# Optimization experiments

Hardware: AMD Instinct MI355X
Metric: run time of the kernel (lower is better)

The kernel has to match this reference:

```python
import jax, jax.numpy as jnp
from jax import lax
import numpy as np

B, T, I, H = 64, 2048, 256, 512


def setup_inputs() -> dict:
    key = jax.random.key(0)
    ks = jax.random.split(key, 5)
    stdv = 1.0 / np.sqrt(H)
    return {
        "x": jax.random.normal(ks[0], (B, T, I), dtype=jnp.float32),
        "w_ih0": jax.random.normal(ks[1], (H, I), dtype=jnp.float32) * 0.01,
        "w_hh0": jax.random.uniform(ks[2], (H,), dtype=jnp.float32, minval=-stdv, maxval=stdv),
        "b_ih0": jnp.zeros((H,), dtype=jnp.float32),
        "w_ih1": jax.random.normal(ks[3], (H, H), dtype=jnp.float32) * 0.01,
        "w_hh1": jax.random.uniform(ks[4], (H,), dtype=jnp.float32, minval=-stdv, maxval=stdv),
        "b_ih1": jnp.zeros((H,), dtype=jnp.float32),
    }


def _indrnn_layer(inp, w_ih, w_hh, b_ih):
    # Precompute input projection for all timesteps in one GEMM
    # (identical math to per-step F.linear). pre: (B, T, H)
    pre = jnp.einsum("bti,hi->bth", inp, w_ih) + b_ih
    h0 = jnp.zeros((inp.shape[0], w_hh.shape[0]), dtype=inp.dtype)

    def step(h, p_t):  # p_t: (B, H)
        h = jax.nn.relu(p_t + w_hh * h)
        return h, h

    _, ys = lax.scan(step, h0, jnp.swapaxes(pre, 0, 1))  # ys: (T, B, H)
    return jnp.swapaxes(ys, 0, 1)  # (B, T, H)


def reference(x, w_ih0, w_hh0, b_ih0, w_ih1, w_hh1, b_ih1):
    out = _indrnn_layer(x, w_ih0, w_hh0, b_ih0)
    out = _indrnn_layer(out, w_ih1, w_hh1, b_ih1)
    return out  # torch module returns (out, None); out.squeeze(2) is a no-op for H>1
```

## Files before the change

kernel.cpp:

```cpp
#include <hip/hip_runtime.h>
#include <hip/hip_bf16.h>


#define BB 64
#define TT 2048
#define II 256
#define HH 512
#define MM (BB * TT)

typedef __attribute__((ext_vector_type(8))) short bf16x8;
typedef __attribute__((ext_vector_type(4))) float f32x4;

__device__ inline unsigned short bf16_rne(float f) {
  unsigned u = __builtin_bit_cast(unsigned, f);
  u += 0x7FFFu + ((u >> 16) & 1u);
  return (unsigned short)(u >> 16);
}
__device__ inline float bf16_val(unsigned short h) {
  unsigned u = ((unsigned)h) << 16;
  return __builtin_bit_cast(float, u);
}

template <int K>
__global__ __launch_bounds__(256) void gemm_mfma(const float* __restrict__ A,
                                                 const float* __restrict__ W,
                                                 const float* __restrict__ bias,
                                                 float* __restrict__ C) {
  constexpr int BM = 128, BN = 128, BK = 32;
  constexpr int LDT = 40;
  __shared__ unsigned short Ah[BM * LDT], Al[BM * LDT];
  __shared__ unsigned short Bh[BN * LDT], Bl[BN * LDT];

  const int bid = blockIdx.x;
  const int xcd = bid & 7;
  const int local = bid >> 3;
  const int mb = xcd * (MM / BM / 8) + (local >> 2);
  const int nb = local & 3;
  const int m0 = mb * BM, n0 = nb * BN;

  const int tid = threadIdx.x;
  const int lane = tid & 63;
  const int wave = tid >> 6;
  const int wr = wave >> 1, wc = wave & 1;
  const int lrow = lane & 15, lkg = lane >> 4;

  f32x4 acc[4][4] = {};

  const int srow = tid >> 1;
  const int skq = (tid & 1) * 4;

  for (int kt = 0; kt < K; kt += BK) {
    const float4* Aq = (const float4*)(A + (size_t)(m0 + srow) * K + kt) + skq;
    const float4* Wq = (const float4*)(W + (size_t)(n0 + srow) * K + kt) + skq;
    float4 av[4], wv[4];
#pragma unroll
    for (int s = 0; s < 4; ++s) { av[s] = Aq[s]; wv[s] = Wq[s]; }

    __syncthreads();

#pragma unroll
    for (int s = 0; s < 4; ++s) {
      const int kk = (skq + s) * 4;
      const float fa[4] = {av[s].x, av[s].y, av[s].z, av[s].w};
      const float fw[4] = {wv[s].x, wv[s].y, wv[s].z, wv[s].w};
      ushort4 ah, al, wh, wl;
      unsigned short* pah = (unsigned short*)&ah;
      unsigned short* pal = (unsigned short*)&al;
      unsigned short* pwh = (unsigned short*)&wh;
      unsigned short* pwl = (unsigned short*)&wl;
#pragma unroll
      for (int e = 0; e < 4; ++e) {
        const unsigned short h1 = bf16_rne(fa[e]);
        pah[e] = h1;
        pal[e] = bf16_rne(fa[e] - bf16_val(h1));
        const unsigned short h2 = bf16_rne(fw[e]);
        pwh[e] = h2;
        pwl[e] = bf16_rne(fw[e] - bf16_val(h2));
      }
      *(ushort4*)&Ah[srow * LDT + kk] = ah;
      *(ushort4*)&Al[srow * LDT + kk] = al;
      *(ushort4*)&Bh[srow * LDT + kk] = wh;
      *(ushort4*)&Bl[srow * LDT + kk] = wl;
    }
    __syncthreads();

    bf16x8 afh[4], afl[4], bfh[4], bfl[4];
#pragma unroll
    for (int i = 0; i < 4; ++i) {
      const int ar = wr * 64 + i * 16 + lrow;
      afh[i] = *(const bf16x8*)&Ah[ar * LDT + lkg * 8];
      afl[i] = *(const bf16x8*)&Al[ar * LDT + lkg * 8];
      const int br = wc * 64 + i * 16 + lrow;
      bfh[i] = *(const bf16x8*)&Bh[br * LDT + lkg * 8];
      bfl[i] = *(const bf16x8*)&Bl[br * LDT + lkg * 8];
    }
#pragma unroll
    for (int i = 0; i < 4; ++i)
#pragma unroll
      for (int j = 0; j < 4; ++j) {
        acc[i][j] = __builtin_amdgcn_mfma_f32_16x16x32_bf16(afh[i], bfh[j], acc[i][j], 0, 0, 0);
        acc[i][j] = __builtin_amdgcn_mfma_f32_16x16x32_bf16(afh[i], bfl[j], acc[i][j], 0, 0, 0);
        acc[i][j] = __builtin_amdgcn_mfma_f32_16x16x32_bf16(afl[i], bfh[j], acc[i][j], 0, 0, 0);
      }
  }

  const int rb = (lane >> 4) * 4;
#pragma unroll
  for (int j = 0; j < 4; ++j) {
    const int col = n0 + wc * 64 + j * 16 + lrow;
    const float bv = bias[col];
#pragma unroll
    for (int i = 0; i < 4; ++i) {
      const int row0 = m0 + wr * 64 + i * 16 + rb;
#pragma unroll
      for (int r = 0; r < 4; ++r)
        C[(size_t)(row0 + r) * HH + col] = acc[i][j][r] + bv;
    }
  }
}

__global__ __launch_bounds__(256, 1) void indrnn_scan(float* __restrict__ buf,
                                                      const float* __restrict__ w_hh) {
  const int gid = blockIdx.x * 256 + threadIdx.x;
  const int b = gid >> 9;
  const int h = gid & 511;
  const float w = w_hh[h];
  float* p = buf + (size_t)b * TT * HH + h;

  constexpr int U = 64;
  float cur[U], nxt[U];
  float hv = 0.f;

#pragma unroll
  for (int u = 0; u < U; ++u) cur[u] = p[(size_t)u * HH];

  for (int t0 = 0; t0 < TT; t0 += U) {
    const bool more = (t0 + U) < TT;
    if (more) {
#pragma unroll
      for (int u = 0; u < U; ++u) nxt[u] = p[(size_t)(t0 + U + u) * HH];
    }
#pragma unroll
    for (int u = 0; u < U; ++u) {
      hv = fmaxf(fmaf(w, hv, cur[u]), 0.f);
      cur[u] = hv;
    }
#pragma unroll
    for (int u = 0; u < U; ++u) p[(size_t)(t0 + u) * HH] = cur[u];
    if (more) {
#pragma unroll
      for (int u = 0; u < U; ++u) cur[u] = nxt[u];
    }
  }
}

extern "C" void kernel_launch(void* const* d_in, const int* in_sizes, int n_in,
                              void* d_out, int out_size, void* d_ws, size_t ws_size,
                              hipStream_t stream) {
  const float* x     = (const float*)d_in[0];
  const float* w_ih0 = (const float*)d_in[1];
  const float* w_hh0 = (const float*)d_in[2];
  const float* b_ih0 = (const float*)d_in[3];
  const float* w_ih1 = (const float*)d_in[4];
  const float* w_hh1 = (const float*)d_in[5];
  const float* b_ih1 = (const float*)d_in[6];
  float* out = (float*)d_out;
  float* ws  = (float*)d_ws;

  const int ntiles = (MM / 128) * (HH / 128);

  gemm_mfma<II><<<ntiles, 256, 0, stream>>>(x, w_ih0, b_ih0, ws);
  indrnn_scan<<<(BB * HH) / 256, 256, 0, stream>>>(ws, w_hh0);
  gemm_mfma<HH><<<ntiles, 256, 0, stream>>>(ws, w_ih1, b_ih1, out);
  indrnn_scan<<<(BB * HH) / 256, 256, 0, stream>>>(out, w_hh1);
}
```

Before: 1.022 ms.

## Pre-split weights and layer-1 activations to bf16 hi/lo; async LDS-prefetch scan

Adds a kernel that converts the weights once into bf16 high/low halves, and makes the first scan emit its output directly as bf16 high/low pairs, so the second GEMM loads pre-split operands instead of converting fp32 in every tile. The scan is rewritten as 64-thread blocks that stream the pre-activations into LDS with global_load_lds and several chunks in flight. This removes the per-tile conversion ALU work and fp32 loads, at the cost of extra workspace, two small launches, and writing two 16-bit arrays instead of one fp32 array. A fallback path runs when the workspace is too small.

```diff
diff --git a/kernel.cpp b/kernel.cpp
--- a/kernel.cpp
+++ b/kernel.cpp
@@ -21,11 +21,18 @@
   return __builtin_bit_cast(float, u);
 }
 
-template <int K>
-__global__ __launch_bounds__(256) void gemm_mfma(const float* __restrict__ A,
-                                                 const float* __restrict__ W,
-                                                 const float* __restrict__ bias,
-                                                 float* __restrict__ C) {
+typedef __attribute__((address_space(1))) const void GASV;
+typedef __attribute__((address_space(3))) void LASV;
+__device__ inline void gload_lds4(const float* g, float* l) {
+  __builtin_amdgcn_global_load_lds((GASV*)g, (LASV*)l, 4, 0, 0);
+}
+
+template <int K, int MODE>
+__global__ __launch_bounds__(256) void gemm_mfma(
+    const float* __restrict__ Af, const unsigned short* __restrict__ Ahg,
+    const unsigned short* __restrict__ Alg, const float* __restrict__ Wf,
+    const unsigned short* __restrict__ Whg, const unsigned short* __restrict__ Wlg,
+    const float* __restrict__ bias, float* __restrict__ C) {
   constexpr int BM = 128, BN = 128, BK = 32;
   constexpr int LDT = 40;
   __shared__ unsigned short Ah[BM * LDT], Al[BM * LDT];
@@ -48,39 +55,81 @@
 
   const int srow = tid >> 1;
   const int skq = (tid & 1) * 4;
+  const int skq8 = (tid & 1) * 16;
 
   for (int kt = 0; kt < K; kt += BK) {
-    const float4* Aq = (const float4*)(A + (size_t)(m0 + srow) * K + kt) + skq;
-    const float4* Wq = (const float4*)(W + (size_t)(n0 + srow) * K + kt) + skq;
     float4 av[4], wv[4];
-#pragma unroll
-    for (int s = 0; s < 4; ++s) { av[s] = Aq[s]; wv[s] = Wq[s]; }
+    bf16x8 a8[4], w8[4];
+    if constexpr (MODE == 2) {
+      const size_t ro = (size_t)(m0 + srow) * K + kt + skq8;
+      a8[0] = *(const bf16x8*)(Ahg + ro);
+      a8[1] = *(const bf16x8*)(Ahg + ro + 8);
+      a8[2] = *(const bf16x8*)(Alg + ro);
+      a8[3] = *(const bf16x8*)(Alg + ro + 8);
+    } else {
+      const float4* Aq = (const float4*)(Af + (size_t)(m0 + srow) * K + kt) + skq;
+#pragma unroll
+      for (int s = 0; s < 4; ++s) av[s] = Aq[s];
+    }
+    if constexpr (MODE >= 1) {
+      const size_t ro = (size_t)(n0 + srow) * K + kt + skq8;
+      w8[0] = *(const bf16x8*)(Whg + ro);
+      w8[1] = *(const bf16x8*)(Whg + ro + 8);
+      w8[2] = *(const bf16x8*)(Wlg + ro);
+      w8[3] = *(const bf16x8*)(Wlg + ro + 8);
+    } else {
+      const float4* Wq = (const float4*)(Wf + (size_t)(n0 + srow) * K + kt) + skq;
+#pragma unroll
+      for (int s = 0; s < 4; ++s) wv[s] = Wq[s];
+    }
 
     __syncthreads();
 
-#pragma unroll
-    for (int s = 0; s < 4; ++s) {
-      const int kk = (skq + s) * 4;
-      const float fa[4] = {av[s].x, av[s].y, av[s].z, av[s].w};
-      const float fw[4] = {wv[s].x, wv[s].y, wv[s].z, wv[s].w};
-      ushort4 ah, al, wh, wl;
-      unsigned short* pah = (unsigned short*)&ah;
-      unsigned short* pal = (unsigned short*)&al;
-      unsigned short* pwh = (unsigned short*)&wh;
-      unsigned short* pwl = (unsigned short*)&wl;
-#pragma unroll
-      for (int e = 0; e < 4; ++e) {
-        const unsigned short h1 = bf16_rne(fa[e]);
-        pah[e] = h1;
-        pal[e] = bf16_rne(fa[e] - bf16_val(h1));
-        const unsigned short h2 = bf16_rne(fw[e]);
-        pwh[e] = h2;
-        pwl[e] = bf16_rne(fw[e] - bf16_val(h2));
-      }
-      *(ushort4*)&Ah[srow * LDT + kk] = ah;
-      *(ushort4*)&Al[srow * LDT + kk] = al;
-      *(ushort4*)&Bh[srow * LDT + kk] = wh;
-      *(ushort4*)&Bl[srow * LDT + kk] = wl;
+    if constexpr (MODE == 2) {
+      *(bf16x8*)&Ah[srow * LDT + skq8] = a8[0];
+      *(bf16x8*)&Ah[srow * LDT + skq8 + 8] = a8[1];
+      *(bf16x8*)&Al[srow * LDT + skq8] = a8[2];
+      *(bf16x8*)&Al[srow * LDT + skq8 + 8] = a8[3];
+    } else {
+#pragma unroll
+      for (int s = 0; s < 4; ++s) {
+        const int kk = (skq + s) * 4;
+        const float fa[4] = {av[s].x, av[s].y, av[s].z, av[s].w};
+        ushort4 ah4, al4;
+        unsigned short* pah = (unsigned short*)&ah4;
+        unsigned short* pal = (unsigned short*)&al4;
+#pragma unroll
+        for (int e = 0; e < 4; ++e) {
+          const unsigned short h1 = bf16_rne(fa[e]);
+          pah[e] = h1;
+          pal[e] = bf16_rne(fa[e] - bf16_val(h1));
+        }
+        *(ushort4*)&Ah[srow * LDT + kk] = ah4;
+        *(ushort4*)&Al[srow * LDT + kk] = al4;
+      }
+    }
+    if constexpr (MODE >= 1) {
+      *(bf16x8*)&Bh[srow * LDT + skq8] = w8[0];
+      *(bf16x8*)&Bh[srow * LDT + skq8 + 8] = w8[1];
+      *(bf16x8*)&Bl[srow * LDT + skq8] = w8[2];
+      *(bf16x8*)&Bl[srow * LDT + skq8 + 8] = w8[3];
+    } else {
+#pragma unroll
+      for (int s = 0; s < 4; ++s) {
+        const int kk = (skq + s) * 4;
+        const float fw[4] = {wv[s].x, wv[s].y, wv[s].z, wv[s].w};
+        ushort4 wh4, wl4;
+        unsigned short* pwh = (unsigned short*)&wh4;
+        unsigned short* pwl = (unsigned short*)&wl4;
+#pragma unroll
+        for (int e = 0; e < 4; ++e) {
+          const unsigned short h2 = bf16_rne(fw[e]);
+          pwh[e] = h2;
+          pwl[e] = bf16_rne(fw[e] - bf16_val(h2));
+        }
+        *(ushort4*)&Bh[srow * LDT + kk] = wh4;
+        *(ushort4*)&Bl[srow * LDT + kk] = wl4;
+      }
     }
     __syncthreads();
 
@@ -119,38 +168,62 @@
   }
 }
 
-__global__ __launch_bounds__(256, 1) void indrnn_scan(float* __restrict__ buf,
-                                                      const float* __restrict__ w_hh) {
-  const int gid = blockIdx.x * 256 + threadIdx.x;
-  const int b = gid >> 9;
-  const int h = gid & 511;
+template <bool SPLIT>
+__global__ __launch_bounds__(64) void indrnn_scan2(
+    const float* __restrict__ pre, const float* __restrict__ w_hh,
+    float* __restrict__ outf, unsigned short* __restrict__ outh,
+    unsigned short* __restrict__ outl) {
+  constexpr int CH = 16, NCH = TT / CH, AHEAD = 3;
+  __shared__ float lds[4 * CH * 64];
+  const int lane = threadIdx.x;
+  const int gid = blockIdx.x * 64 + lane;
+  const int h = gid & (HH - 1);
+  const size_t colbase = (size_t)(gid >> 9) * TT * HH + h;
+
   const float w = w_hh[h];
-  float* p = buf + (size_t)b * TT * HH + h;
-
-  constexpr int U = 64;
-  float cur[U], nxt[U];
   float hv = 0.f;
 
-#pragma unroll
-  for (int u = 0; u < U; ++u) cur[u] = p[(size_t)u * HH];
-
-  for (int t0 = 0; t0 < TT; t0 += U) {
-    const bool more = (t0 + U) < TT;
-    if (more) {
-#pragma unroll
-      for (int u = 0; u < U; ++u) nxt[u] = p[(size_t)(t0 + U + u) * HH];
-    }
-#pragma unroll
-    for (int u = 0; u < U; ++u) {
-      hv = fmaxf(fmaf(w, hv, cur[u]), 0.f);
-      cur[u] = hv;
-    }
-#pragma unroll
-    for (int u = 0; u < U; ++u) p[(size_t)(t0 + u) * HH] = cur[u];
-    if (more) {
-#pragma unroll
-      for (int u = 0; u < U; ++u) cur[u] = nxt[u];
-    }
+  auto issue = [&](int c) {
+    const float* g = pre + colbase + (size_t)(c * CH) * HH;
+    float* l = &lds[(c & 3) * CH * 64];
+#pragma unroll
+    for (int tt = 0; tt < CH; ++tt) gload_lds4(g + (size_t)tt * HH, l + tt * 64);
+  };
+
+  issue(0);
+  issue(1);
+  issue(2);
+  for (int c = 0; c < NCH; ++c) {
+    if (c + AHEAD < NCH) issue(c + AHEAD);
+    asm volatile("s_waitcnt vmcnt(48)" ::: "memory");
+    __builtin_amdgcn_sched_barrier(0);
+    const float* l = &lds[(c & 3) * CH * 64];
+#pragma unroll
+    for (int tt = 0; tt < CH; ++tt) {
+      const float p = l[tt * 64 + lane];
+      hv = fmaxf(fmaf(w, hv, p), 0.f);
+      const size_t gi = colbase + (size_t)(c * CH + tt) * HH;
+      if constexpr (SPLIT) {
+        const unsigned short hh = bf16_rne(hv);
+        outh[gi] = hh;
+        outl[gi] = bf16_rne(hv - bf16_val(hh));
+      } else {
+        outf[gi] = hv;
+      }
+    }
+  }
+}
+
+__global__ __launch_bounds__(256) void convert_w(const float* __restrict__ W,
+                                                 unsigned short* __restrict__ Wh,
+                                                 unsigned short* __restrict__ Wl,
+                                                 int n) {
+  const int i = blockIdx.x * 256 + threadIdx.x;
+  if (i < n) {
+    const float f = W[i];
+    const unsigned short hh = bf16_rne(f);
+    Wh[i] = hh;
+    Wl[i] = bf16_rne(f - bf16_val(hh));
   }
 }
 
@@ -165,12 +238,37 @@
   const float* w_hh1 = (const float*)d_in[5];
   const float* b_ih1 = (const float*)d_in[6];
   float* out = (float*)d_out;
-  float* ws  = (float*)d_ws;
+  float* pre0 = (float*)d_ws;
+  char* wsb = (char*)d_ws;
+
+  const size_t OFF_A1H = 268435456ull;
+  const size_t OFF_A1L = OFF_A1H + 134217728ull;
+  const size_t OFF_W0H = OFF_A1L + 134217728ull;
+  const size_t OFF_W0L = OFF_W0H + 262144ull;
+  const size_t OFF_W1H = OFF_W0L + 262144ull;
+  const size_t OFF_W1L = OFF_W1H + 524288ull;
+  const size_t NEED = OFF_W1L + 524288ull;
 
   const int ntiles = (MM / 128) * (HH / 128);
 
-  gemm_mfma<II><<<ntiles, 256, 0, stream>>>(x, w_ih0, b_ih0, ws);
-  indrnn_scan<<<(BB * HH) / 256, 256, 0, stream>>>(ws, w_hh0);
-  gemm_mfma<HH><<<ntiles, 256, 0, stream>>>(ws, w_ih1, b_ih1, out);
-  indrnn_scan<<<(BB * HH) / 256, 256, 0, stream>>>(out, w_hh1);
-}
+  if (ws_size >= NEED) {
+    unsigned short* A1h = (unsigned short*)(wsb + OFF_A1H);
+    unsigned short* A1l = (unsigned short*)(wsb + OFF_A1L);
+    unsigned short* W0h = (unsigned short*)(wsb + OFF_W0H);
+    unsigned short* W0l = (unsigned short*)(wsb + OFF_W0L);
+    unsigned short* W1h = (unsigned short*)(wsb + OFF_W1H);
+    unsigned short* W1l = (unsigned short*)(wsb + OFF_W1L);
+
+    convert_w<<<(HH * II) / 256, 256, 0, stream>>>(w_ih0, W0h, W0l, HH * II);
+    convert_w<<<(HH * HH) / 256, 256, 0, stream>>>(w_ih1, W1h, W1l, HH * HH);
+    gemm_mfma<II, 1><<<ntiles, 256, 0, stream>>>(x, nullptr, nullptr, nullptr, W0h, W0l, b_ih0, pre0);
+    indrnn_scan2<true><<<(BB * HH) / 64, 64, 0, stream>>>(pre0, w_hh0, nullptr, A1h, A1l);
+    gemm_mfma<HH, 2><<<ntiles, 256, 0, stream>>>(nullptr, A1h, A1l, nullptr, W1h, W1l, b_ih1, out);
+    indrnn_scan2<false><<<(BB * HH) / 64, 64, 0, stream>>>(out, w_hh1, out, nullptr, nullptr);
+  } else {
+    gemm_mfma<II, 0><<<ntiles, 256, 0, stream>>>(x, nullptr, nullptr, w_ih0, nullptr, nullptr, b_ih0, pre0);
+    indrnn_scan2<false><<<(BB * HH) / 64, 64, 0, stream>>>(pre0, w_hh0, pre0, nullptr, nullptr);
+    gemm_mfma<HH, 0><<<ntiles, 256, 0, stream>>>(pre0, nullptr, nullptr, w_ih1, nullptr, nullptr, b_ih1, out);
+    indrnn_scan2<false><<<(BB * HH) / 64, 64, 0, stream>>>(out, w_hh1, out, nullptr, nullptr);
+  }
+}
```

New measurement: 944.4 us. 7.6% less time.
